# Kernel optimization log

Measured on AMD Instinct MI355X. Metric: run time of the kernel, lower is better.

## Reference

```python
import jax, jax.numpy as jnp
import numpy as np

B, S, D_IN, D_OUT, H = 2, 2048, 1024, 1024, 16
HD = D_OUT // H

def setup_inputs() -> dict:
    key = jax.random.key(0)
    ks = jax.random.split(key, 6)
    sc_in = 1.0 / np.sqrt(D_IN)
    sc_out = 1.0 / np.sqrt(D_OUT)
    return {
        "x": jax.random.normal(ks[0], (B, S, D_IN), dtype=jnp.float32),
        "Wq": jax.random.uniform(ks[1], (D_IN, D_OUT), jnp.float32, -sc_in, sc_in),
        "Wk": jax.random.uniform(ks[2], (D_IN, D_OUT), jnp.float32, -sc_in, sc_in),
        "Wv": jax.random.uniform(ks[3], (D_IN, D_OUT), jnp.float32, -sc_in, sc_in),
        "Wo": jax.random.uniform(ks[4], (D_OUT, D_OUT), jnp.float32, -sc_out, sc_out),
        "bo": jax.random.uniform(ks[5], (D_OUT,), jnp.float32, -sc_out, sc_out),
    }

def reference(x, Wq, Wk, Wv, Wo, bo):
    b, s, _ = x.shape
    # QKV projections (no bias), split heads -> [b, h, s, hd]
    q = (x @ Wq).reshape(b, s, H, HD).transpose(0, 2, 1, 3)
    k = (x @ Wk).reshape(b, s, H, HD).transpose(0, 2, 1, 3)
    v = (x @ Wv).reshape(b, s, H, HD).transpose(0, 2, 1, 3)
    scores = jnp.einsum('bhqd,bhkd->bhqk', q, k)
    causal = jnp.triu(jnp.ones((s, s), dtype=bool), k=1)
    scores = jnp.where(causal, -jnp.inf, scores)
    w = jax.nn.softmax(scores / np.sqrt(HD), axis=-1)  # dropout p=0.0 -> identity
    ctx = jnp.einsum('bhqk,bhkd->bhqd', w, v)
    ctx = ctx.transpose(0, 2, 1, 3).reshape(b, s, D_OUT)
    return ctx @ Wo + bo
```

## Files before the change

kernel.cpp:

```cpp
#include <hip/hip_runtime.h>
#include <stdint.h>

typedef unsigned short u16;
typedef __attribute__((ext_vector_type(8))) short short8;
typedef __attribute__((ext_vector_type(4))) float floatx4;
typedef __attribute__((ext_vector_type(4))) u16 ushort4v;

typedef __attribute__((address_space(1))) const uint32_t gu32;
typedef __attribute__((address_space(3))) uint32_t lu32;

#define MFMA(a, b, c) __builtin_amdgcn_mfma_f32_16x16x32_bf16((a), (b), (c), 0, 0, 0)

#define QSCALE 0.1803368801111204f

__device__ __forceinline__ u16 f2bf(float f) {
    union { float f; uint32_t u; } x; x.f = f;
    uint32_t u = x.u;
    u += 0x7fffu + ((u >> 16) & 1u);
    return (u16)(u >> 16);
}

__device__ __forceinline__ uint32_t pack_trunc(float hi, float lo) {
    return __builtin_amdgcn_perm(__float_as_uint(hi), __float_as_uint(lo), 0x07060302u);
}

__device__ __forceinline__ void async16(u16* lds, const u16* g) {
    __builtin_amdgcn_global_load_lds((gu32*)g, (lu32*)lds, 16, 0, 0);
}

__global__ __launch_bounds__(256) void prep_kernel(
    const float* __restrict__ x,
    const float* __restrict__ W0, const float* __restrict__ W1,
    const float* __restrict__ W2, const float* __restrict__ W3,
    u16* __restrict__ WT, u16* __restrict__ Xbf)
{
    const int z = blockIdx.z;
    const int tx = threadIdx.x, ty = threadIdx.y;
    if (z == 4) {
        const int bid = blockIdx.y * 32 + blockIdx.x;
        const int t = ty * 32 + tx;
        const size_t base = ((size_t)bid * 256 + t) * 16;
        const float* xf = x + base;
        short8 v0, v1;
#pragma unroll
        for (int j = 0; j < 8; j++) v0[j] = (short)f2bf(xf[j]);
#pragma unroll
        for (int j = 0; j < 8; j++) v1[j] = (short)f2bf(xf[8 + j]);
        *(short8*)&Xbf[base] = v0;
        *(short8*)&Xbf[base + 8] = v1;
        return;
    }
    __shared__ u16 tile[32][33];
    const float* W = (z == 0) ? W0 : (z == 1) ? W1 : (z == 2) ? W2 : W3;
    u16* dst = WT + (size_t)z * 1024 * 1024;
    const int n0 = blockIdx.x * 32, k0 = blockIdx.y * 32;
#pragma unroll
    for (int i = 0; i < 4; i++)
        tile[ty + i * 8][tx] = f2bf(W[(size_t)(k0 + ty + i * 8) * 1024 + n0 + tx]);
    __syncthreads();
#pragma unroll
    for (int i = 0; i < 4; i++)
        dst[(size_t)(n0 + ty + i * 8) * 1024 + k0 + tx] = tile[tx][ty + i * 8];
}

__global__ __launch_bounds__(256) void gemm_qkv_kernel(
    const u16* __restrict__ X, const u16* __restrict__ WT,
    u16* __restrict__ Q, u16* __restrict__ Kout, u16* __restrict__ VT)
{
    __shared__ __align__(16) u16 As[128 * 32];
    __shared__ __align__(16) u16 Bs[128 * 32];
    const int bid = blockIdx.x;
    const int xcd = bid & 7;
    const int idx = bid >> 3;
    const int mat = idx >> 5;
    const int rr  = (idx >> 3) & 3;
    const int nn  = idx & 7;
    const int m0 = (xcd * 4 + rr) * 128;
    const int n0 = nn * 128;
    const u16* BW = WT + (size_t)mat * 1024 * 1024;
    const int tid = threadIdx.x;
    const int wave = tid >> 6, lane = tid & 63;
    const int lrow = lane & 15, lquad = lane >> 4;
    const int wr = (wave >> 1) * 64, wc = (wave & 1) * 64;

    const int ci0 = wave * 128 + lane;
    const int ci1 = ci0 + 64;
    const int ar0 = ci0 >> 2, ac0 = (ci0 & 3) * 8;
    const int ar1 = ci1 >> 2, ac1 = (ci1 & 3) * 8;
    u16* ldsA0 = As + (size_t)(wave * 128) * 8;
    u16* ldsA1 = As + (size_t)(wave * 128 + 64) * 8;
    u16* ldsB0 = Bs + (size_t)(wave * 128) * 8;
    u16* ldsB1 = Bs + (size_t)(wave * 128 + 64) * 8;
    const u16* gA0 = &X[(size_t)(m0 + ar0) * 1024 + ac0];
    const u16* gA1 = &X[(size_t)(m0 + ar1) * 1024 + ac1];
    const u16* gB0 = &BW[(size_t)(n0 + ar0) * 1024 + ac0];
    const u16* gB1 = &BW[(size_t)(n0 + ar1) * 1024 + ac1];

    floatx4 acc[4][4];
#pragma unroll
    for (int mt = 0; mt < 4; mt++)
#pragma unroll
        for (int nt = 0; nt < 4; nt++) acc[mt][nt] = (floatx4){0.f, 0.f, 0.f, 0.f};

    for (int k0 = 0; k0 < 1024; k0 += 32) {
        __syncthreads();
        async16(ldsA0, gA0 + k0);
        async16(ldsA1, gA1 + k0);
        async16(ldsB0, gB0 + k0);
        async16(ldsB1, gB1 + k0);
        __syncthreads();
        short8 af[4], bf[4];
#pragma unroll
        for (int mt = 0; mt < 4; mt++)
            af[mt] = *(const short8*)&As[(wr + mt * 16 + lrow) * 32 + lquad * 8];
#pragma unroll
        for (int nt = 0; nt < 4; nt++)
            bf[nt] = *(const short8*)&Bs[(wc + nt * 16 + lrow) * 32 + lquad * 8];
#pragma unroll
        for (int mt = 0; mt < 4; mt++)
#pragma unroll
            for (int nt = 0; nt < 4; nt++)
                acc[mt][nt] = MFMA(af[mt], bf[nt], acc[mt][nt]);
    }

#pragma unroll
    for (int mt = 0; mt < 4; mt++) {
        const int gm = m0 + wr + mt * 16 + lquad * 4;
        const int b_ = gm >> 11;
        const int s  = gm & 2047;
        const int kt = s >> 6;
        const int r  = s & 63;
#pragma unroll
        for (int nt = 0; nt < 4; nt++) {
            const int gn = n0 + wc + nt * 16 + lrow;
            const int h = gn >> 6, hd = gn & 63;
            const int bh = b_ * 16 + h;
            if (mat == 2) {
                const size_t base = ((size_t)(bh * 32 + kt) * 64 + hd) * 64
                                  + ((((r >> 3) ^ (hd & 7)) << 3) | (r & 7));
                ushort4v v;
#pragma unroll
                for (int i = 0; i < 4; i++) v[i] = f2bf(acc[mt][nt][i]);
                *(ushort4v*)&VT[base] = v;
            } else if (mat == 1) {
#pragma unroll
                for (int i = 0; i < 4; i++) {
                    const int r2 = r + i;
                    Kout[((size_t)(bh * 32 + kt) * 64 + r2) * 64
                         + (((hd >> 3) ^ (r2 & 7)) << 3) + (hd & 7)] = f2bf(acc[mt][nt][i]);
                }
            } else {
#pragma unroll
                for (int i = 0; i < 4; i++)
                    Q[((size_t)bh * 2048 + s + i) * 64 + hd] = f2bf(acc[mt][nt][i] * QSCALE);
            }
        }
    }
}

__global__ __launch_bounds__(256, 4) void attn_kernel(
    const u16* __restrict__ Q, const u16* __restrict__ Ksw,
    const u16* __restrict__ Vsw, u16* __restrict__ ctx)
{
    __shared__ __align__(16) u16 Ks[2][4096];
    __shared__ __align__(16) u16 Vs[2][4096];
    __shared__ __align__(16) u16 P[4][1024];
    const int tid = threadIdx.x, wave = tid >> 6, lane = tid & 63;
    const int lrow = lane & 15, lquad = lane >> 4;
    const float NEGINF = -__builtin_inff();

    const int bh = blockIdx.x & 31;
    const int g = blockIdx.x >> 5;
    const int qb = (g < 16) ? (31 - g) : (g - 16);
    const int ntiles = qb + 1;
    const int q0 = qb * 64 + wave * 16;

    const u16* Qb = Q   + (size_t)bh * 2048 * 64;
    const u16* Kt = Ksw + (size_t)bh * 32 * 4096;
    const u16* Vt = Vsw + (size_t)bh * 32 * 4096;

    const short8 qf0 = *(const short8*)&Qb[(size_t)(q0 + lrow) * 64 + lquad * 8];
    const short8 qf1 = *(const short8*)&Qb[(size_t)(q0 + lrow) * 64 + 32 + lquad * 8];

    const int r7 = lrow & 7;
    int koff0[4], koff1[4], voff[2][4];
#pragma unroll
    for (int nt = 0; nt < 4; nt++) {
        const int row = nt * 16 + lrow;
        koff0[nt] = row * 64 + ((lquad ^ r7) << 3);
        koff1[nt] = row * 64 + (((4 + lquad) ^ r7) << 3);
    }
#pragma unroll
    for (int st = 0; st < 2; st++)
#pragma unroll
        for (int ht = 0; ht < 4; ht++) {
            const int row = ht * 16 + lrow;
            voff[st][ht] = row * 64 + (((st * 4 + lquad) ^ r7) << 3);
        }
    int pwoff[4], proff[2];
#pragma unroll
    for (int nt = 0; nt < 4; nt++)
        pwoff[nt] = lrow * 64 + (((nt * 2 + (lquad >> 1)) ^ r7) << 3) + ((lquad & 1) << 2);
#pragma unroll
    for (int st = 0; st < 2; st++)
        proff[st] = lrow * 64 + (((st * 4 + lquad) ^ r7) << 3);

    const int myq = q0 + lrow;
    float m_s = NEGINF, l_s = 0.f;
    floatx4 o[4];
#pragma unroll
    for (int i = 0; i < 4; i++) o[i] = (floatx4){0.f, 0.f, 0.f, 0.f};

    const int co0 = wave * 1024;
    const int co1 = wave * 1024 + 512;
    const int lo8 = lane * 8;

    async16(&Ks[0][co0], Kt + co0 + lo8);
    async16(&Ks[0][co1], Kt + co1 + lo8);
    async16(&Vs[0][co0], Vt + co0 + lo8);
    async16(&Vs[0][co1], Vt + co1 + lo8);

    u16* Pw = P[wave];

    for (int kt = 0; kt < ntiles; kt++) {
        __syncthreads();
        if (kt + 1 < ntiles) {
            const u16* Kn = Kt + (size_t)(kt + 1) * 4096;
            const u16* Vn = Vt + (size_t)(kt + 1) * 4096;
            const int nb = (kt + 1) & 1;
            async16(&Ks[nb][co0], Kn + co0 + lo8);
            async16(&Ks[nb][co1], Kn + co1 + lo8);
            async16(&Vs[nb][co0], Vn + co0 + lo8);
            async16(&Vs[nb][co1], Vn + co1 + lo8);
        }
        const u16* kbuf = Ks[kt & 1];
        const u16* vbuf = Vs[kt & 1];

        floatx4 s[4];
#pragma unroll
        for (int nt = 0; nt < 4; nt++) {
            const short8 kf0 = *(const short8*)&kbuf[koff0[nt]];
            const short8 kf1 = *(const short8*)&kbuf[koff1[nt]];
            floatx4 a = (floatx4){0.f, 0.f, 0.f, 0.f};
            a = MFMA(kf0, qf0, a);
            a = MFMA(kf1, qf1, a);
            s[nt] = a;
        }

        const bool diag = (kt == ntiles - 1);
        if (diag) {
#pragma unroll
            for (int nt = 0; nt < 4; nt++)
#pragma unroll
                for (int i = 0; i < 4; i++)
                    if (kt * 64 + nt * 16 + lquad * 4 + i > myq) s[nt][i] = NEGINF;
        }
        float mx = NEGINF;
#pragma unroll
        for (int nt = 0; nt < 4; nt++)
#pragma unroll
            for (int i = 0; i < 4; i++) mx = fmaxf(mx, s[nt][i]);
        mx = fmaxf(mx, __shfl_xor(mx, 16));
        mx = fmaxf(mx, __shfl_xor(mx, 32));
        const float mnew = fmaxf(m_s, mx);
        const float alpha = exp2f(m_s - mnew);
        m_s = mnew;
        float sum = 0.f;
#pragma unroll
        for (int nt = 0; nt < 4; nt++)
#pragma unroll
            for (int i = 0; i < 4; i++) {
                const float pv = exp2f(s[nt][i] - mnew);
                s[nt][i] = pv;
                sum += pv;
            }
        sum += __shfl_xor(sum, 16);
        sum += __shfl_xor(sum, 32);
        l_s = l_s * alpha + sum;
#pragma unroll
        for (int ht = 0; ht < 4; ht++)
#pragma unroll
            for (int i = 0; i < 4; i++) o[ht][i] *= alpha;

#pragma unroll
        for (int nt = 0; nt < 4; nt++) {
            uint2 pk;
            pk.x = pack_trunc(s[nt][1], s[nt][0]);
            pk.y = pack_trunc(s[nt][3], s[nt][2]);
            *(uint2*)&Pw[pwoff[nt]] = pk;
        }
#pragma unroll
        for (int st = 0; st < 2; st++) {
            const short8 pf = *(const short8*)&Pw[proff[st]];
#pragma unroll
            for (int ht = 0; ht < 4; ht++) {
                const short8 vf = *(const short8*)&vbuf[voff[st][ht]];
                o[ht] = MFMA(vf, pf, o[ht]);
            }
        }
    }

    const int b_ = bh >> 4, h_ = bh & 15;
    const float inv_l = 1.0f / l_s;
#pragma unroll
    for (int ht = 0; ht < 4; ht++) {
        uint32_t pk0 = (uint32_t)f2bf(o[ht][0] * inv_l) | ((uint32_t)f2bf(o[ht][1] * inv_l) << 16);
        uint32_t pk1 = (uint32_t)f2bf(o[ht][2] * inv_l) | ((uint32_t)f2bf(o[ht][3] * inv_l) << 16);
        uint2 pk = {pk0, pk1};
        *(uint2*)&ctx[((size_t)(b_ * 2048 + q0 + lrow)) * 1024 + h_ * 64 + ht * 16 + lquad * 4] = pk;
    }
}

__global__ __launch_bounds__(256) void gemm_out_kernel(
    const u16* __restrict__ X, const u16* __restrict__ WT,
    const float* __restrict__ bias, float* __restrict__ out)
{
    __shared__ __align__(16) u16 As[128 * 32];
    __shared__ __align__(16) u16 Bs[128 * 32];
    const int bid = blockIdx.x;
    const int xcd = bid & 7;
    const int idx = bid >> 3;
    const int rr  = idx >> 3;
    const int nn  = idx & 7;
    const int m0 = (xcd * 4 + rr) * 128;
    const int n0 = nn * 128;
    const int tid = threadIdx.x;
    const int wave = tid >> 6, lane = tid & 63;
    const int lrow = lane & 15, lquad = lane >> 4;
    const int wr = (wave >> 1) * 64, wc = (wave & 1) * 64;

    const int ci0 = wave * 128 + lane;
    const int ci1 = ci0 + 64;
    const int ar0 = ci0 >> 2, ac0 = (ci0 & 3) * 8;
    const int ar1 = ci1 >> 2, ac1 = (ci1 & 3) * 8;
    u16* ldsA0 = As + (size_t)(wave * 128) * 8;
    u16* ldsA1 = As + (size_t)(wave * 128 + 64) * 8;
    u16* ldsB0 = Bs + (size_t)(wave * 128) * 8;
    u16* ldsB1 = Bs + (size_t)(wave * 128 + 64) * 8;
    const u16* gA0 = &X[(size_t)(m0 + ar0) * 1024 + ac0];
    const u16* gA1 = &X[(size_t)(m0 + ar1) * 1024 + ac1];
    const u16* gB0 = &WT[(size_t)(n0 + ar0) * 1024 + ac0];
    const u16* gB1 = &WT[(size_t)(n0 + ar1) * 1024 + ac1];

    floatx4 acc[4][4];
#pragma unroll
    for (int mt = 0; mt < 4; mt++)
#pragma unroll
        for (int nt = 0; nt < 4; nt++) acc[mt][nt] = (floatx4){0.f, 0.f, 0.f, 0.f};

    for (int k0 = 0; k0 < 1024; k0 += 32) {
        __syncthreads();
        async16(ldsA0, gA0 + k0);
        async16(ldsA1, gA1 + k0);
        async16(ldsB0, gB0 + k0);
        async16(ldsB1, gB1 + k0);
        __syncthreads();
        short8 af[4], bf[4];
#pragma unroll
        for (int mt = 0; mt < 4; mt++)
            af[mt] = *(const short8*)&As[(wr + mt * 16 + lrow) * 32 + lquad * 8];
#pragma unroll
        for (int nt = 0; nt < 4; nt++)
            bf[nt] = *(const short8*)&Bs[(wc + nt * 16 + lrow) * 32 + lquad * 8];
#pragma unroll
        for (int mt = 0; mt < 4; mt++)
#pragma unroll
            for (int nt = 0; nt < 4; nt++)
                acc[mt][nt] = MFMA(af[mt], bf[nt], acc[mt][nt]);
    }

#pragma unroll
    for (int mt = 0; mt < 4; mt++) {
        const int gm = m0 + wr + mt * 16 + lquad * 4;
#pragma unroll
        for (int nt = 0; nt < 4; nt++) {
            const int gn = n0 + wc + nt * 16 + lrow;
            const float bv = bias[gn];
#pragma unroll
            for (int i = 0; i < 4; i++)
                out[(size_t)(gm + i) * 1024 + gn] = acc[mt][nt][i] + bv;
        }
    }
}

extern "C" void kernel_launch(void* const* d_in, const int* in_sizes, int n_in,
                              void* d_out, int out_size, void* d_ws, size_t ws_size,
                              hipStream_t stream) {
    u16* ws = (u16*)d_ws + 64;

    const size_t MB1 = 1024 * 1024;
    u16* WT   = ws;
    u16* Qw   = ws + 4 * MB1;
    u16* Kw   = ws + 8 * MB1;
    u16* VTw  = ws + 12 * MB1;
    u16* ctxw = ws + 16 * MB1;
    u16* Xbf  = ws + 20 * MB1;

    prep_kernel<<<dim3(32, 32, 5), dim3(32, 8), 0, stream>>>(
        (const float*)d_in[0], (const float*)d_in[1], (const float*)d_in[2],
        (const float*)d_in[3], (const float*)d_in[4], WT, Xbf);
    gemm_qkv_kernel<<<768, 256, 0, stream>>>(Xbf, WT, Qw, Kw, VTw);
    attn_kernel<<<1024, 256, 0, stream>>>(Qw, Kw, VTw, ctxw);
    gemm_out_kernel<<<256, 256, 0, stream>>>(ctxw, WT + 3 * MB1, (const float*)d_in[5], (float*)d_out);
}
```

Before: 197.8 us.

## Pre-swizzle GEMM operand layouts in global memory to avoid LDS bank conflicts

Stores X, the transposed weights and the attention context in global memory with 8-element chunks XOR-permuted within each 32-column group, keyed on row bits. The GEMM kernels copy these straight into LDS and read fragments at the matching swizzled offset. This is meant to remove LDS bank conflicts on the 16-byte fragment reads without changing the direct global-to-LDS copy path. The cost is that producers and consumers must agree on one layout, and the context stores become slightly less contiguous.

Result: no change. 195.4 us (-1.2%).

```diff
diff --git a/kernel.cpp b/kernel.cpp
--- a/kernel.cpp
+++ b/kernel.cpp
@@ -27,6 +27,7 @@
 __device__ __forceinline__ void async16(u16* lds, const u16* g) {
     __builtin_amdgcn_global_load_lds((gu32*)g, (lu32*)lds, 16, 0, 0);
 }
+
 
 __global__ __launch_bounds__(256) void prep_kernel(
     const float* __restrict__ x,
@@ -40,14 +41,20 @@
         const int bid = blockIdx.y * 32 + blockIdx.x;
         const int t = ty * 32 + tx;
         const size_t base = ((size_t)bid * 256 + t) * 16;
+        const int row = (int)(base >> 10);
+        const int col0 = (int)(base & 1023);
+        const int key = (row >> 1) & 3;
+        const int grp = col0 & ~31;
+        const int c0 = (col0 >> 3) & 3;
         const float* xf = x + base;
         short8 v0, v1;
 #pragma unroll
         for (int j = 0; j < 8; j++) v0[j] = (short)f2bf(xf[j]);
 #pragma unroll
         for (int j = 0; j < 8; j++) v1[j] = (short)f2bf(xf[8 + j]);
-        *(short8*)&Xbf[base] = v0;
-        *(short8*)&Xbf[base + 8] = v1;
+        u16* dr = Xbf + (size_t)row * 1024 + grp;
+        *(short8*)&dr[(c0 ^ key) << 3] = v0;
+        *(short8*)&dr[((c0 + 1) ^ key) << 3] = v1;
         return;
     }
     __shared__ u16 tile[32][33];
@@ -59,8 +66,12 @@
         tile[ty + i * 8][tx] = f2bf(W[(size_t)(k0 + ty + i * 8) * 1024 + n0 + tx]);
     __syncthreads();
 #pragma unroll
-    for (int i = 0; i < 4; i++)
-        dst[(size_t)(n0 + ty + i * 8) * 1024 + k0 + tx] = tile[tx][ty + i * 8];
+    for (int i = 0; i < 4; i++) {
+        const int n = n0 + ty + i * 8;
+        const int key = (n >> 1) & 3;
+        const int sc = k0 + (((((tx >> 3) & 3) ^ key)) << 3) + (tx & 7);
+        dst[(size_t)n * 1024 + sc] = tile[tx][ty + i * 8];
+    }
 }
 
 __global__ __launch_bounds__(256) void gemm_qkv_kernel(
@@ -82,6 +93,7 @@
     const int wave = tid >> 6, lane = tid & 63;
     const int lrow = lane & 15, lquad = lane >> 4;
     const int wr = (wave >> 1) * 64, wc = (wave & 1) * 64;
+    const int fragoff = ((lquad ^ ((lrow >> 1) & 3)) << 3);
 
     const int ci0 = wave * 128 + lane;
     const int ci1 = ci0 + 64;
@@ -112,10 +124,10 @@
         short8 af[4], bf[4];
 #pragma unroll
         for (int mt = 0; mt < 4; mt++)
-            af[mt] = *(const short8*)&As[(wr + mt * 16 + lrow) * 32 + lquad * 8];
+            af[mt] = *(const short8*)&As[(wr + mt * 16 + lrow) * 32 + fragoff];
 #pragma unroll
         for (int nt = 0; nt < 4; nt++)
-            bf[nt] = *(const short8*)&Bs[(wc + nt * 16 + lrow) * 32 + lquad * 8];
+            bf[nt] = *(const short8*)&Bs[(wc + nt * 16 + lrow) * 32 + fragoff];
 #pragma unroll
         for (int mt = 0; mt < 4; mt++)
 #pragma unroll
@@ -302,12 +314,16 @@
 
     const int b_ = bh >> 4, h_ = bh & 15;
     const float inv_l = 1.0f / l_s;
+    const int skey = (lrow >> 1) & 3;
 #pragma unroll
     for (int ht = 0; ht < 4; ht++) {
         uint32_t pk0 = (uint32_t)f2bf(o[ht][0] * inv_l) | ((uint32_t)f2bf(o[ht][1] * inv_l) << 16);
         uint32_t pk1 = (uint32_t)f2bf(o[ht][2] * inv_l) | ((uint32_t)f2bf(o[ht][3] * inv_l) << 16);
         uint2 pk = {pk0, pk1};
-        *(uint2*)&ctx[((size_t)(b_ * 2048 + q0 + lrow)) * 1024 + h_ * 64 + ht * 16 + lquad * 4] = pk;
+        const int col = h_ * 64 + ((ht >> 1) << 5)
+                      + (((((ht & 1) << 1) | (lquad >> 1)) ^ skey) << 3)
+                      + ((lquad & 1) << 2);
+        *(uint2*)&ctx[((size_t)(b_ * 2048 + q0 + lrow)) * 1024 + col] = pk;
     }
 }
 
@@ -328,6 +344,7 @@
     const int wave = tid >> 6, lane = tid & 63;
     const int lrow = lane & 15, lquad = lane >> 4;
     const int wr = (wave >> 1) * 64, wc = (wave & 1) * 64;
+    const int fragoff = ((lquad ^ ((lrow >> 1) & 3)) << 3);
 
     const int ci0 = wave * 128 + lane;
     const int ci1 = ci0 + 64;
@@ -358,10 +375,10 @@
         short8 af[4], bf[4];
 #pragma unroll
         for (int mt = 0; mt < 4; mt++)
-            af[mt] = *(const short8*)&As[(wr + mt * 16 + lrow) * 32 + lquad * 8];
+            af[mt] = *(const short8*)&As[(wr + mt * 16 + lrow) * 32 + fragoff];
 #pragma unroll
         for (int nt = 0; nt < 4; nt++)
-            bf[nt] = *(const short8*)&Bs[(wc + nt * 16 + lrow) * 32 + lquad * 8];
+            bf[nt] = *(const short8*)&Bs[(wc + nt * 16 + lrow) * 32 + fragoff];
 #pragma unroll
         for (int mt = 0; mt < 4; mt++)
 #pragma unroll
```
